# Kernel tuning notes

Measured on AMD Instinct MI355X. Metric: run time of the kernel, lower is better.

Reference implementation:

```python
import jax, jax.numpy as jnp
import numpy as np

B, S, D = 4, 2048, 2048
NQ, NKV = 16, 4
HD = D // NQ          # head_size = 128
GROUP = NQ // NKV     # 4


def _rope_table(seq_len, head_size, theta=10000.0):
    # [seq, head_size/2, 2] = (cos, sin), matching torch polar freqs_cis
    inv = 1.0 / (theta ** (np.arange(0, head_size, 2, dtype=np.float32) / head_size))
    ang = np.arange(seq_len, dtype=np.float32)[:, None] * inv[None, :]
    return jnp.asarray(np.stack([np.cos(ang), np.sin(ang)], axis=-1))


def setup_inputs() -> dict:
    key = jax.random.key(0)
    ks = jax.random.split(key, 6)
    sd = 0.02
    return {
        "x": jax.random.normal(ks[0], (B, S, D), jnp.float32),
        "freq_cis": _rope_table(S, HD),
        "Wq": jax.random.normal(ks[1], (D, NQ * HD), jnp.float32) * sd,
        "bq": jnp.zeros((NQ * HD,), jnp.float32),
        "Wk": jax.random.normal(ks[2], (D, NKV * HD), jnp.float32) * sd,
        "bk": jnp.zeros((NKV * HD,), jnp.float32),
        "Wv": jax.random.normal(ks[3], (D, NKV * HD), jnp.float32) * sd,
        "bv": jnp.zeros((NKV * HD,), jnp.float32),
        "Wo": jax.random.normal(ks[4], (NQ * HD, D), jnp.float32) * sd,
        "start_pos": 0,
    }


def _apply_rope(x, fc):
    # x: [b, s, h, d]; fc: [s, d/2, 2] -> complex multiply on (even, odd) pairs
    xr = x.reshape(*x.shape[:-1], -1, 2)
    cos = fc[None, :, None, :, 0]
    sin = fc[None, :, None, :, 1]
    x0, x1 = xr[..., 0], xr[..., 1]
    out = jnp.stack([x0 * cos - x1 * sin, x0 * sin + x1 * cos], axis=-1)
    return out.reshape(x.shape)


def reference(x, freq_cis, Wq, bq, Wk, bk, Wv, bv, Wo, start_pos):
    b, s, _ = x.shape
    q = (x @ Wq + bq).reshape(b, s, NQ, HD)
    k = (x @ Wk + bk).reshape(b, s, NKV, HD)
    v = (x @ Wv + bv).reshape(b, s, NKV, HD)

    fc = freq_cis[start_pos:start_pos + s]
    q = _apply_rope(q, fc)
    k = _apply_rope(k, fc)

    # [b, nkv, group, s, d] query view; k/v stay [b, nkv, s, d] (GQA broadcast)
    q = q.transpose(0, 2, 1, 3).reshape(b, NKV, GROUP, s, HD)
    k = k.transpose(0, 2, 1, 3)
    v = v.transpose(0, 2, 1, 3)

    scale = 1.0 / jnp.sqrt(jnp.asarray(HD, x.dtype))
    scores = jnp.einsum("bhgqd,bhkd->bhgqk", q, k) * scale
    causal = jnp.tril(jnp.ones((s, s), bool))
    scores = jnp.where(causal[None, None, None], scores, jnp.asarray(-jnp.inf, scores.dtype))
    probs = jax.nn.softmax(scores, axis=-1)
    o = jnp.einsum("bhgqk,bhkd->bhgqd", probs, v)

    o = o.reshape(b, NQ, s, HD).transpose(0, 2, 1, 3).reshape(b, s, NQ * HD)
    return o @ Wo
```

## Files before the change

kernel.cpp:

```cpp
#include <hip/hip_runtime.h>
#include <stdint.h>

typedef __attribute__((ext_vector_type(8))) short bf16x8;
typedef __attribute__((ext_vector_type(4))) float f32x4;
typedef __attribute__((ext_vector_type(16))) float f32x16;

#define S_LEN 2048
#define D_MODEL 2048
#define NQH 16
#define NKVH 4
#define HDIM 128
#define BATCH 4

__device__ __forceinline__ float bf2f(unsigned short s) {
  union { unsigned u; float f; } v; v.u = ((unsigned)s) << 16; return v.f;
}
__device__ __forceinline__ unsigned short f2bf(float f) {
  union { float f; unsigned u; } v; v.f = f;
  unsigned r = v.u + 0x7FFFu + ((v.u >> 16) & 1u);
  return (unsigned short)(r >> 16);
}
__device__ __forceinline__ f32x4 fzero() {
  f32x4 v; v[0]=0.f; v[1]=0.f; v[2]=0.f; v[3]=0.f; return v;
}
__device__ __forceinline__ void async16(const void* g, void* l) {
  __builtin_amdgcn_global_load_lds(
      (const __attribute__((address_space(1))) unsigned int*)g,
      (__attribute__((address_space(3))) unsigned int*)l, 16, 0, 0);
}
__device__ __forceinline__ unsigned cvtpk(float lo, float hi) {
  unsigned r;
  asm("v_cvt_pk_bf16_f32 %0, %1, %2" : "=v"(r) : "v"(lo), "v"(hi));
  return r;
}

__global__ void k_convert_x(const float* __restrict__ x, unsigned short* __restrict__ xb, int n4) {
  int stride = gridDim.x * blockDim.x;
  for (int i = blockIdx.x * blockDim.x + threadIdx.x; i < n4; i += stride) {
    float4 v = ((const float4*)x)[i];
    ushort4 o;
    o.x = f2bf(v.x); o.y = f2bf(v.y); o.z = f2bf(v.z); o.w = f2bf(v.w);
    ((ushort4*)xb)[i] = o;
  }
}

__global__ void k_transpose_convert(const float* __restrict__ W, unsigned short* __restrict__ Wt,
                                    int K, int N) {
  __shared__ float tile[32][33];
  int tx = threadIdx.x & 31, ty = threadIdx.x >> 5;
  int n0 = blockIdx.x * 32, k0 = blockIdx.y * 32;
  #pragma unroll
  for (int i = 0; i < 4; ++i)
    tile[ty + i*8][tx] = W[(size_t)(k0 + ty + i*8) * N + n0 + tx];
  __syncthreads();
  #pragma unroll
  for (int i = 0; i < 4; ++i)
    Wt[(size_t)(n0 + ty + i*8) * K + k0 + tx] = f2bf(tile[tx][ty + i*8]);
}

__global__ void k_transpose_bf16(const unsigned short* __restrict__ src,
                                 unsigned short* __restrict__ dst, int R, int C) {
  __shared__ unsigned short tile[32][33];
  int tx = threadIdx.x & 31, ty = threadIdx.x >> 5;
  int c0 = blockIdx.x * 32, r0 = blockIdx.y * 32;
  const unsigned short* s = src + (size_t)blockIdx.z * R * C;
  unsigned short* d = dst + (size_t)blockIdx.z * R * C;
  #pragma unroll
  for (int i = 0; i < 4; ++i)
    tile[ty + i*8][tx] = s[(size_t)(r0 + ty + i*8) * C + c0 + tx];
  __syncthreads();
  #pragma unroll
  for (int i = 0; i < 4; ++i)
    d[(size_t)(c0 + ty + i*8) * R + r0 + tx] = tile[tx][ty + i*8];
}

__global__ void k_rope(unsigned short* __restrict__ T, const float* __restrict__ fc,
                       const int* __restrict__ start_pos, int total) {
  int sp = start_pos[0];
  int stride = gridDim.x * blockDim.x;
  for (int i = blockIdx.x * blockDim.x + threadIdx.x; i < total; i += stride) {
    int d2 = i & 63;
    int s = (i >> 6) & (S_LEN - 1);
    unsigned v = ((const unsigned*)T)[i];
    float x0 = bf2f((unsigned short)(v & 0xFFFFu));
    float x1 = bf2f((unsigned short)(v >> 16));
    float c  = fc[((size_t)(sp + s) * 64 + d2) * 2];
    float sn = fc[((size_t)(sp + s) * 64 + d2) * 2 + 1];
    float y0 = x0 * c - x1 * sn;
    float y1 = x0 * sn + x1 * c;
    ((unsigned*)T)[i] = (unsigned)f2bf(y0) | ((unsigned)f2bf(y1) << 16);
  }
}

__global__ __launch_bounds__(256) void k_gemm_qkv(
    const unsigned short* __restrict__ A, const unsigned short* __restrict__ Bt,
    const float* __restrict__ bq, const float* __restrict__ bk, const float* __restrict__ bv,
    unsigned short* __restrict__ Qo, unsigned short* __restrict__ Ko, unsigned short* __restrict__ Vo)
{
  const int Kdim = 2048;
  __shared__ unsigned short As[128 * 64];
  __shared__ unsigned short Bs[128 * 64];
  const int tid = threadIdx.x;
  const int lane = tid & 63, wave = tid >> 6;
  const int lr = lane & 15, g = lane >> 4;
  const int wm = wave >> 1, wn = wave & 1;
  const int mbase = blockIdx.y * 128;
  const int nbase = blockIdx.x * 128;

  f32x4 acc[4][4];
  #pragma unroll
  for (int mr = 0; mr < 4; ++mr)
    #pragma unroll
    for (int nr = 0; nr < 4; ++nr) acc[mr][nr] = fzero();

  for (int kt = 0; kt < Kdim / 64; ++kt) {
    #pragma unroll
    for (int it = 0; it < 4; ++it) {
      int c = tid + it * 256;
      int row = c >> 3, col = c & 7;
      int lcol = col ^ (row & 7);
      async16(A + (size_t)(mbase + row) * Kdim + kt * 64 + lcol * 8, &As[c * 8]);
    }
    #pragma unroll
    for (int it = 0; it < 4; ++it) {
      int c = tid + it * 256;
      int row = c >> 3, col = c & 7;
      int lcol = col ^ (row & 7);
      async16(Bt + (size_t)(nbase + row) * Kdim + kt * 64 + lcol * 8, &Bs[c * 8]);
    }
    __syncthreads();
    #pragma unroll
    for (int kc = 0; kc < 2; ++kc) {
      bf16x8 af[4], bfr[4];
      int Xl = kc * 64 + g * 16;
      #pragma unroll
      for (int mr = 0; mr < 4; ++mr) {
        int row = wm * 64 + mr * 16 + lr;
        int Xs = Xl ^ ((row & 7) << 4);
        af[mr] = *(const bf16x8*)&As[row * 64 + Xs / 2];
      }
      #pragma unroll
      for (int nr = 0; nr < 4; ++nr) {
        int row = wn * 64 + nr * 16 + lr;
        int Xs = Xl ^ ((row & 7) << 4);
        bfr[nr] = *(const bf16x8*)&Bs[row * 64 + Xs / 2];
      }
      #pragma unroll
      for (int mr = 0; mr < 4; ++mr)
        #pragma unroll
        for (int nr = 0; nr < 4; ++nr)
          acc[mr][nr] = __builtin_amdgcn_mfma_f32_16x16x32_bf16(af[mr], bfr[nr], acc[mr][nr], 0, 0, 0);
    }
    __syncthreads();
  }

  #pragma unroll
  for (int mr = 0; mr < 4; ++mr)
    #pragma unroll
    for (int nr = 0; nr < 4; ++nr)
      #pragma unroll
      for (int i = 0; i < 4; ++i) {
        int m = mbase + wm * 64 + mr * 16 + g * 4 + i;
        int n = nbase + wn * 64 + nr * 16 + lr;
        int b = m >> 11, s = m & 2047;
        float val = acc[mr][nr][i];
        if (n < 2048) {
          val += bq[n];
          int h = n >> 7, d = n & 127;
          Qo[((size_t)(b * NQH + h) * S_LEN + s) * HDIM + d] = f2bf(val);
        } else if (n < 2560) {
          int nn = n - 2048;
          val += bk[nn];
          int h = nn >> 7, d = nn & 127;
          Ko[((size_t)(b * NKVH + h) * S_LEN + s) * HDIM + d] = f2bf(val);
        } else {
          int nn = n - 2560;
          val += bv[nn];
          int h = nn >> 7, d = nn & 127;
          Vo[((size_t)(b * NKVH + h) * S_LEN + s) * HDIM + d] = f2bf(val);
        }
      }
}

__global__ __launch_bounds__(256) void k_gemm_out(
    const unsigned short* __restrict__ A, const unsigned short* __restrict__ Bt,
    float* __restrict__ C)
{
  const int Kdim = 2048;
  __shared__ unsigned short As[128 * 64];
  __shared__ unsigned short Bs[128 * 64];
  const int tid = threadIdx.x;
  const int lane = tid & 63, wave = tid >> 6;
  const int lr = lane & 15, g = lane >> 4;
  const int wm = wave >> 1, wn = wave & 1;
  const int mbase = blockIdx.y * 128;
  const int nbase = blockIdx.x * 128;

  f32x4 acc[4][4];
  #pragma unroll
  for (int mr = 0; mr < 4; ++mr)
    #pragma unroll
    for (int nr = 0; nr < 4; ++nr) acc[mr][nr] = fzero();

  for (int kt = 0; kt < Kdim / 64; ++kt) {
    #pragma unroll
    for (int it = 0; it < 4; ++it) {
      int c = tid + it * 256;
      int row = c >> 3, col = c & 7;
      int lcol = col ^ (row & 7);
      async16(A + (size_t)(mbase + row) * Kdim + kt * 64 + lcol * 8, &As[c * 8]);
    }
    #pragma unroll
    for (int it = 0; it < 4; ++it) {
      int c = tid + it * 256;
      int row = c >> 3, col = c & 7;
      int lcol = col ^ (row & 7);
      async16(Bt + (size_t)(nbase + row) * Kdim + kt * 64 + lcol * 8, &Bs[c * 8]);
    }
    __syncthreads();
    #pragma unroll
    for (int kc = 0; kc < 2; ++kc) {
      bf16x8 af[4], bfr[4];
      int Xl = kc * 64 + g * 16;
      #pragma unroll
      for (int mr = 0; mr < 4; ++mr) {
        int row = wm * 64 + mr * 16 + lr;
        int Xs = Xl ^ ((row & 7) << 4);
        af[mr] = *(const bf16x8*)&As[row * 64 + Xs / 2];
      }
      #pragma unroll
      for (int nr = 0; nr < 4; ++nr) {
        int row = wn * 64 + nr * 16 + lr;
        int Xs = Xl ^ ((row & 7) << 4);
        bfr[nr] = *(const bf16x8*)&Bs[row * 64 + Xs / 2];
      }
      #pragma unroll
      for (int mr = 0; mr < 4; ++mr)
        #pragma unroll
        for (int nr = 0; nr < 4; ++nr)
          acc[mr][nr] = __builtin_amdgcn_mfma_f32_16x16x32_bf16(af[mr], bfr[nr], acc[mr][nr], 0, 0, 0);
    }
    __syncthreads();
  }

  #pragma unroll
  for (int mr = 0; mr < 4; ++mr)
    #pragma unroll
    for (int nr = 0; nr < 4; ++nr)
      #pragma unroll
      for (int i = 0; i < 4; ++i) {
        int m = mbase + wm * 64 + mr * 16 + g * 4 + i;
        int n = nbase + wn * 64 + nr * 16 + lr;
        C[(size_t)m * 2048 + n] = acc[mr][nr][i];
      }
}

__global__ __launch_bounds__(512, 2) void k_flash2(
    const unsigned short* __restrict__ Q, const unsigned short* __restrict__ K,
    const unsigned short* __restrict__ Vt, unsigned short* __restrict__ O)
{
  __shared__ __align__(16) unsigned short SH[32768];

  const int tid = threadIdx.x;
  const int lane = tid & 63;
  const int w = tid >> 6;
  const int ql = lane & 31;
  const int hi = lane >> 5;

  const int bh = blockIdx.x >> 2;
  const int tp = blockIdx.x & 3;
  const int b = bh >> 4, h = bh & 15;
  const int kh = h >> 2;

  const unsigned short* Qbase = Q + (size_t)(b * NQH + h) * S_LEN * HDIM;
  const unsigned short* Kbase = K + (size_t)(b * NKVH + kh) * S_LEN * HDIM;
  const unsigned short* Vtb   = Vt + (size_t)(b * NKVH + kh) * HDIM * S_LEN;

  const float scale = 0.08838834764831845f;

  #pragma unroll 1
  for (int half = 0; half < 2; ++half) {
    const int t = half ? (7 - tp) : tp;
    const int nkv = 4 * t + 4;
    const int qg = t * 256 + w * 32 + ql;

    __syncthreads();

    bf16x8 qf[8];
    {
      const unsigned short* qp = Qbase + (size_t)qg * HDIM;
      #pragma unroll
      for (int dd = 0; dd < 8; ++dd)
        qf[dd] = *(const bf16x8*)(qp + dd * 16 + hi * 8);
    }

    float m_r = -1e30f, l_r = 0.f;
    f32x16 oA[4];
    #pragma unroll
    for (int db = 0; db < 4; ++db)
      #pragma unroll
      for (int r = 0; r < 16; ++r) oA[db][r] = 0.f;

    {
      unsigned short* Kd = SH;
      unsigned short* Vd = SH + 16384;
      #pragma unroll
      for (int it = 0; it < 2; ++it) {
        int c = tid + it * 512;
        int row = c >> 4, col = c & 15;
        int lcol = (col & 8) | ((col ^ (row & 7)) & 7);
        async16(Kbase + (size_t)row * HDIM + lcol * 8, Kd + c * 8);
      }
      #pragma unroll
      for (int it = 0; it < 2; ++it) {
        int c = tid + it * 512;
        int row = c >> 3, col = c & 7;
        int lcol = col ^ (row & 7);
        async16(Vtb + (size_t)row * S_LEN + lcol * 8, Vd + c * 8);
      }
    }
    __syncthreads();

    for (int j = 0; j < nkv; ++j) {
      const int cur = j & 1;
      const unsigned short* Kl = SH + cur * 8192;
      const unsigned short* Vl = SH + 16384 + cur * 8192;

      if (j + 1 < nkv) {
        unsigned short* Kd = SH + (cur ^ 1) * 8192;
        unsigned short* Vd = SH + 16384 + (cur ^ 1) * 8192;
        #pragma unroll
        for (int it = 0; it < 2; ++it) {
          int c = tid + it * 512;
          int row = c >> 4, col = c & 15;
          int lcol = (col & 8) | ((col ^ (row & 7)) & 7);
          async16(Kbase + (size_t)((j + 1) * 64 + row) * HDIM + lcol * 8, Kd + c * 8);
        }
        #pragma unroll
        for (int it = 0; it < 2; ++it) {
          int c = tid + it * 512;
          int row = c >> 3, col = c & 7;
          int lcol = col ^ (row & 7);
          async16(Vtb + (size_t)row * S_LEN + (j + 1) * 64 + lcol * 8, Vd + c * 8);
        }
      }

      if (j * 64 <= t * 256 + w * 32 + 31) {
        f32x16 p0, p1;
        #pragma unroll
        for (int r = 0; r < 16; ++r) { p0[r] = 0.f; p1[r] = 0.f; }
        #pragma unroll
        for (int dd = 0; dd < 8; ++dd) {
          const int off = (((dd * 32 + hi * 16) ^ ((ql & 7) << 4)) >> 1);
          bf16x8 a0 = *(const bf16x8*)&Kl[ql * 128 + off];
          bf16x8 a1 = *(const bf16x8*)&Kl[(32 + ql) * 128 + off];
          p0 = __builtin_amdgcn_mfma_f32_32x32x16_bf16(a0, qf[dd], p0, 0, 0, 0);
          p1 = __builtin_amdgcn_mfma_f32_32x32x16_bf16(a1, qf[dd], p1, 0, 0, 0);
        }

        #pragma unroll
        for (int r = 0; r < 16; ++r) {
          const int kl = (r & 3) + 8 * (r >> 2);
          int kg = j * 64 + kl + 4 * hi;
          p0[r] = (kg > qg) ? -1e30f : p0[r] * scale;
          p1[r] = (kg + 32 > qg) ? -1e30f : p1[r] * scale;
        }

        float pm = -1e30f;
        #pragma unroll
        for (int r = 0; r < 16; ++r) pm = fmaxf(pm, fmaxf(p0[r], p1[r]));
        pm = fmaxf(pm, __shfl_xor(pm, 32));
        const float mn = fmaxf(m_r, pm);
        const float corr = __expf(m_r - mn);
        m_r = mn;
        float rs = 0.f;
        #pragma unroll
        for (int r = 0; r < 16; ++r) {
          p0[r] = __expf(p0[r] - mn);
          p1[r] = __expf(p1[r] - mn);
          rs += p0[r] + p1[r];
        }
        rs += __shfl_xor(rs, 32);
        l_r = l_r * corr + rs;
        #pragma unroll
        for (int db = 0; db < 4; ++db)
          #pragma unroll
          for (int r = 0; r < 16; ++r) oA[db][r] *= corr;

        bf16x8 pb[4];
        {
          unsigned Wv[8], W2v[8];
          #pragma unroll
          for (int d = 0; d < 4; ++d) {
            Wv[d]      = cvtpk(p0[4*d],     p0[4*d + 1]);
            W2v[d]     = cvtpk(p0[4*d + 2], p0[4*d + 3]);
            Wv[4 + d]  = cvtpk(p1[4*d],     p1[4*d + 1]);
            W2v[4 + d] = cvtpk(p1[4*d + 2], p1[4*d + 3]);
          }
          #pragma unroll
          for (int kt = 0; kt < 2; ++kt) {
            #pragma unroll
            for (int s = 0; s < 2; ++s) {
              unsigned ownW   = hi ? Wv[kt*4 + 2*s + 1]  : Wv[kt*4 + 2*s];
              unsigned sendW  = hi ? Wv[kt*4 + 2*s]      : Wv[kt*4 + 2*s + 1];
              unsigned recvW  = (unsigned)__shfl_xor((int)sendW, 32);
              unsigned ownW2  = hi ? W2v[kt*4 + 2*s + 1] : W2v[kt*4 + 2*s];
              unsigned sendW2 = hi ? W2v[kt*4 + 2*s]     : W2v[kt*4 + 2*s + 1];
              unsigned recvW2 = (unsigned)__shfl_xor((int)sendW2, 32);
              union { unsigned u[4]; bf16x8 v; } pk;
              pk.u[0] = hi ? recvW  : ownW;
              pk.u[1] = hi ? recvW2 : ownW2;
              pk.u[2] = hi ? ownW   : recvW;
              pk.u[3] = hi ? ownW2  : recvW2;
              pb[kt*2 + s] = pk.v;
            }
          }
        }

        #pragma unroll
        for (int ks = 0; ks < 4; ++ks) {
          #pragma unroll
          for (int db = 0; db < 4; ++db) {
            const int off = (((ks * 32 + hi * 16) ^ ((ql & 7) << 4)) >> 1);
            bf16x8 av = *(const bf16x8*)&Vl[(db * 32 + ql) * 64 + off];
            oA[db] = __builtin_amdgcn_mfma_f32_32x32x16_bf16(av, pb[ks], oA[db], 0, 0, 0);
          }
        }
      }
      __syncthreads();
    }

    {
      const float invl = 1.f / l_r;
      const int qloc = w * 32 + ql;
      #pragma unroll
      for (int db = 0; db < 4; ++db)
        #pragma unroll
        for (int g4 = 0; g4 < 4; ++g4) {
          unsigned lo  = cvtpk(oA[db][g4*4 + 0] * invl, oA[db][g4*4 + 1] * invl);
          unsigned hi2 = cvtpk(oA[db][g4*4 + 2] * invl, oA[db][g4*4 + 3] * invl);
          int byteoff = qloc * 256 + ((db * 64 + g4 * 16 + hi * 8) ^ ((qloc & 7) << 4));
          *(uint2*)((char*)SH + byteoff) = make_uint2(lo, hi2);
        }
    }
    __syncthreads();
    {
      const int q2 = tid >> 1, hf = tid & 1;
      unsigned short* orow = O + ((size_t)(b * S_LEN + t * 256 + q2)) * D_MODEL + h * HDIM + hf * 64;
      #pragma unroll
      for (int u = 0; u < 8; ++u) {
        int byteoff = q2 * 256 + ((hf * 128 + u * 16) ^ ((q2 & 7) << 4));
        bf16x8 v = *(const bf16x8*)((const char*)SH + byteoff);
        *(bf16x8*)(orow + u * 8) = v;
      }
    }
  }
}

extern "C" void kernel_launch(void* const* d_in, const int* in_sizes, int n_in,
                              void* d_out, int out_size, void* d_ws, size_t ws_size,
                              hipStream_t stream) {
  (void)in_sizes; (void)n_in; (void)out_size; (void)ws_size;
  const float* x  = (const float*)d_in[0];
  const float* fc = (const float*)d_in[1];
  const float* Wq = (const float*)d_in[2];
  const float* bq = (const float*)d_in[3];
  const float* Wk = (const float*)d_in[4];
  const float* bk = (const float*)d_in[5];
  const float* Wv = (const float*)d_in[6];
  const float* bv = (const float*)d_in[7];
  const float* Wo = (const float*)d_in[8];
  const int* start_pos = (const int*)d_in[9];
  float* out = (float*)d_out;

  unsigned short* ws = (unsigned short*)d_ws;
  size_t off = 0;
  unsigned short* xb  = ws + off; off += (size_t)8192 * 2048;
  unsigned short* Wt  = ws + off; off += (size_t)3072 * 2048;
  unsigned short* Wot = ws + off; off += (size_t)2048 * 2048;
  unsigned short* Qb  = ws + off; off += (size_t)BATCH * NQH  * S_LEN * HDIM;
  unsigned short* Kb  = ws + off; off += (size_t)BATCH * NKVH * S_LEN * HDIM;
  unsigned short* Vb  = ws + off; off += (size_t)BATCH * NKVH * S_LEN * HDIM;
  unsigned short* Vtb = ws + off; off += (size_t)BATCH * NKVH * S_LEN * HDIM;
  unsigned short* Ob  = ws + off; off += (size_t)8192 * 2048;

  k_convert_x<<<2048, 256, 0, stream>>>(x, xb, 8192 * 2048 / 4);
  k_transpose_convert<<<dim3(64, 64), 256, 0, stream>>>(Wq, Wt, 2048, 2048);
  k_transpose_convert<<<dim3(16, 64), 256, 0, stream>>>(Wk, Wt + (size_t)2048 * 2048, 2048, 512);
  k_transpose_convert<<<dim3(16, 64), 256, 0, stream>>>(Wv, Wt + (size_t)2560 * 2048, 2048, 512);
  k_transpose_convert<<<dim3(64, 64), 256, 0, stream>>>(Wo, Wot, 2048, 2048);

  k_gemm_qkv<<<dim3(24, 64), 256, 0, stream>>>(xb, Wt, bq, bk, bv, Qb, Kb, Vb);

  k_rope<<<2048, 256, 0, stream>>>(Qb, fc, start_pos, BATCH * NQH * S_LEN * 64);
  k_rope<<<2048, 256, 0, stream>>>(Kb, fc, start_pos, BATCH * NKVH * S_LEN * 64);
  k_transpose_bf16<<<dim3(4, 64, 16), 256, 0, stream>>>(Vb, Vtb, S_LEN, HDIM);

  k_flash2<<<dim3(256), 512, 0, stream>>>(Qb, Kb, Vtb, Ob);

  k_gemm_out<<<dim3(16, 64), 256, 0, stream>>>(Ob, Wot, out);
}
```

Measured before the change: 398.2 us.

## Replace QKV and output GEMMs with 256x256 double-buffered pipelined GEMM

Replaces both 128x128 single-buffered GEMM kernels with one templated 256x256-tile kernel using 8 waves. It double-buffers LDS and splits each K-step into four quarter phases that interleave async global-to-LDS staging with MFMA work, using manual waitcnt, barriers and setprio. It also remaps block IDs so neighbouring workgroups share A/B tiles in cache. Larger tiles raise data reuse but leave fewer workgroups (384 and 256) to fill the CUs. The hand-written wait counts are fragile and could race if they are wrong.

```diff
diff --git a/kernel.cpp b/kernel.cpp
--- a/kernel.cpp
+++ b/kernel.cpp
@@ -92,167 +92,181 @@
   }
 }
 
-__global__ __launch_bounds__(256) void k_gemm_qkv(
+
+__device__ __forceinline__ bf16x8 ldsrd(const unsigned short* L, int row, int kk, int g) {
+  int Xs = (kk * 64 + g * 16) ^ ((row & 7) << 4);
+  return *(const bf16x8*)&L[row * 64 + (Xs >> 1)];
+}
+__device__ __forceinline__ void stage8(const unsigned short* __restrict__ G, int gbase,
+                                       int k0, unsigned short* lds, int rowbase, int lane) {
+  int row = rowbase + (lane >> 3);
+  int col8 = (lane & 7) ^ ((lane >> 3) & 7);
+  async16(G + (size_t)(gbase + row) * 2048 + k0 + col8 * 8, lds + rowbase * 64 + lane * 8);
+}
+
+#define BARRIER() __builtin_amdgcn_s_barrier()
+#define LGKM0()  do { asm volatile("s_waitcnt lgkmcnt(0)" ::: "memory"); \
+                      __builtin_amdgcn_sched_barrier(0); } while (0)
+#define VMCNT4() asm volatile("s_waitcnt vmcnt(4)" ::: "memory")
+
+template<int EPI>
+__global__ __launch_bounds__(512, 2) void k_gemm256(
     const unsigned short* __restrict__ A, const unsigned short* __restrict__ Bt,
     const float* __restrict__ bq, const float* __restrict__ bk, const float* __restrict__ bv,
-    unsigned short* __restrict__ Qo, unsigned short* __restrict__ Ko, unsigned short* __restrict__ Vo)
+    unsigned short* __restrict__ Qo, unsigned short* __restrict__ Ko, unsigned short* __restrict__ Vo,
+    float* __restrict__ Cf, int NXT)
 {
-  const int Kdim = 2048;
-  __shared__ unsigned short As[128 * 64];
-  __shared__ unsigned short Bs[128 * 64];
-  const int tid = threadIdx.x;
-  const int lane = tid & 63, wave = tid >> 6;
+  __shared__ __align__(16) unsigned short Abuf[2][256 * 64];
+  __shared__ __align__(16) unsigned short Bbuf[2][256 * 64];
+  const int NT = 32;
+  const int tid = threadIdx.x, lane = tid & 63, w = tid >> 6;
   const int lr = lane & 15, g = lane >> 4;
-  const int wm = wave >> 1, wn = wave & 1;
-  const int mbase = blockIdx.y * 128;
-  const int nbase = blockIdx.x * 128;
-
-  f32x4 acc[4][4];
+  const int wm = w >> 2, wn = w & 3;
+
+  int nwg = NXT * 32;
+  int cpx = nwg >> 3;
+  int bid = blockIdx.x;
+  int swz = (bid & 7) * cpx + (bid >> 3);
+  const int by = swz / NXT, bx = swz % NXT;
+  const int mbase = by * 256, nbase = bx * 256;
+
+  #define ST_AQ02(tt) if ((tt) < NT) { unsigned short* L = Abuf[(tt) & 1]; int k0 = (tt) * 64; \
+    _Pragma("unroll") for (int it = 0; it < 2; ++it) { int sub = it * 8 + w; \
+      stage8(A, mbase, k0, L, (sub >> 3) * 128 + (sub & 7) * 8, lane); } }
+  #define ST_AQ13(tt) if ((tt) < NT) { unsigned short* L = Abuf[(tt) & 1]; int k0 = (tt) * 64; \
+    _Pragma("unroll") for (int it = 0; it < 2; ++it) { int sub = it * 8 + w; \
+      stage8(A, mbase, k0, L, 64 + (sub >> 3) * 128 + (sub & 7) * 8, lane); } }
+  #define ST_BS0(tt) if ((tt) < NT) { unsigned short* L = Bbuf[(tt) & 1]; int k0 = (tt) * 64; \
+    _Pragma("unroll") for (int it = 0; it < 2; ++it) { int sub = it * 8 + w; \
+      stage8(Bt, nbase, k0, L, (sub >> 2) * 64 + (sub & 3) * 8, lane); } }
+  #define ST_BS1(tt) if ((tt) < NT) { unsigned short* L = Bbuf[(tt) & 1]; int k0 = (tt) * 64; \
+    _Pragma("unroll") for (int it = 0; it < 2; ++it) { int sub = it * 8 + w; \
+      stage8(Bt, nbase, k0, L, 32 + (sub >> 2) * 64 + (sub & 3) * 8, lane); } }
+
+  f32x4 acc[8][4];
   #pragma unroll
-  for (int mr = 0; mr < 4; ++mr)
-    #pragma unroll
-    for (int nr = 0; nr < 4; ++nr) acc[mr][nr] = fzero();
-
-  for (int kt = 0; kt < Kdim / 64; ++kt) {
-    #pragma unroll
-    for (int it = 0; it < 4; ++it) {
-      int c = tid + it * 256;
-      int row = c >> 3, col = c & 7;
-      int lcol = col ^ (row & 7);
-      async16(A + (size_t)(mbase + row) * Kdim + kt * 64 + lcol * 8, &As[c * 8]);
+  for (int m = 0; m < 8; ++m)
+    #pragma unroll
+    for (int n = 0; n < 4; ++n) acc[m][n] = fzero();
+
+  ST_AQ02(0); ST_AQ13(0); ST_BS0(0); ST_BS1(0);
+  ST_AQ02(1); ST_BS1(1);
+  VMCNT4();
+  BARRIER();
+
+  bf16x8 a[2][4], b[2][2];
+
+  for (int t = 0; t < NT; ++t) {
+    const unsigned short* Al = Abuf[t & 1];
+    const unsigned short* Bl = Bbuf[t & 1];
+
+    #pragma unroll
+    for (int kk = 0; kk < 2; ++kk) {
+      #pragma unroll
+      for (int m = 0; m < 4; ++m) a[kk][m] = ldsrd(Al, wm * 128 + m * 16 + lr, kk, g);
+      #pragma unroll
+      for (int n = 0; n < 2; ++n) b[kk][n] = ldsrd(Bl, wn * 64 + n * 16 + lr, kk, g);
     }
-    #pragma unroll
-    for (int it = 0; it < 4; ++it) {
-      int c = tid + it * 256;
-      int row = c >> 3, col = c & 7;
-      int lcol = col ^ (row & 7);
-      async16(Bt + (size_t)(nbase + row) * Kdim + kt * 64 + lcol * 8, &Bs[c * 8]);
-    }
-    __syncthreads();
-    #pragma unroll
-    for (int kc = 0; kc < 2; ++kc) {
-      bf16x8 af[4], bfr[4];
-      int Xl = kc * 64 + g * 16;
-      #pragma unroll
-      for (int mr = 0; mr < 4; ++mr) {
-        int row = wm * 64 + mr * 16 + lr;
-        int Xs = Xl ^ ((row & 7) << 4);
-        af[mr] = *(const bf16x8*)&As[row * 64 + Xs / 2];
+    ST_AQ13(t + 1);
+    BARRIER(); LGKM0();
+    __builtin_amdgcn_s_setprio(1);
+    #pragma unroll
+    for (int kk = 0; kk < 2; ++kk)
+      #pragma unroll
+      for (int m = 0; m < 4; ++m)
+        #pragma unroll
+        for (int n = 0; n < 2; ++n)
+          acc[m][n] = __builtin_amdgcn_mfma_f32_16x16x32_bf16(a[kk][m], b[kk][n], acc[m][n], 0, 0, 0);
+    __builtin_amdgcn_s_setprio(0);
+    BARRIER();
+
+    #pragma unroll
+    for (int kk = 0; kk < 2; ++kk)
+      #pragma unroll
+      for (int n = 0; n < 2; ++n) b[kk][n] = ldsrd(Bl, wn * 64 + (2 + n) * 16 + lr, kk, g);
+    ST_BS0(t + 1);
+    BARRIER(); LGKM0();
+    __builtin_amdgcn_s_setprio(1);
+    #pragma unroll
+    for (int kk = 0; kk < 2; ++kk)
+      #pragma unroll
+      for (int m = 0; m < 4; ++m)
+        #pragma unroll
+        for (int n = 0; n < 2; ++n)
+          acc[m][2 + n] = __builtin_amdgcn_mfma_f32_16x16x32_bf16(a[kk][m], b[kk][n], acc[m][2 + n], 0, 0, 0);
+    __builtin_amdgcn_s_setprio(0);
+    BARRIER();
+
+    #pragma unroll
+    for (int kk = 0; kk < 2; ++kk)
+      #pragma unroll
+      for (int m = 0; m < 4; ++m) a[kk][m] = ldsrd(Al, wm * 128 + 64 + m * 16 + lr, kk, g);
+    ST_AQ02(t + 2);
+    BARRIER(); LGKM0();
+    __builtin_amdgcn_s_setprio(1);
+    #pragma unroll
+    for (int kk = 0; kk < 2; ++kk)
+      #pragma unroll
+      for (int m = 0; m < 4; ++m)
+        #pragma unroll
+        for (int n = 0; n < 2; ++n)
+          acc[4 + m][2 + n] = __builtin_amdgcn_mfma_f32_16x16x32_bf16(a[kk][m], b[kk][n], acc[4 + m][2 + n], 0, 0, 0);
+    __builtin_amdgcn_s_setprio(0);
+    BARRIER();
+
+    #pragma unroll
+    for (int kk = 0; kk < 2; ++kk)
+      #pragma unroll
+      for (int n = 0; n < 2; ++n) b[kk][n] = ldsrd(Bl, wn * 64 + n * 16 + lr, kk, g);
+    ST_BS1(t + 2);
+    VMCNT4();
+    BARRIER(); LGKM0();
+    __builtin_amdgcn_s_setprio(1);
+    #pragma unroll
+    for (int kk = 0; kk < 2; ++kk)
+      #pragma unroll
+      for (int m = 0; m < 4; ++m)
+        #pragma unroll
+        for (int n = 0; n < 2; ++n)
+          acc[4 + m][n] = __builtin_amdgcn_mfma_f32_16x16x32_bf16(a[kk][m], b[kk][n], acc[4 + m][n], 0, 0, 0);
+    __builtin_amdgcn_s_setprio(0);
+    BARRIER();
+  }
+
+  #pragma unroll
+  for (int m = 0; m < 8; ++m)
+    #pragma unroll
+    for (int n = 0; n < 4; ++n)
+      #pragma unroll
+      for (int i = 0; i < 4; ++i) {
+        int mg = mbase + wm * 128 + m * 16 + g * 4 + i;
+        int ng = nbase + wn * 64 + n * 16 + lr;
+        float val = acc[m][n][i];
+        if (EPI == 1) {
+          Cf[(size_t)mg * 2048 + ng] = val;
+        } else {
+          int bb = mg >> 11, s = mg & 2047;
+          if (ng < 2048) {
+            val += bq[ng];
+            int h = ng >> 7, d = ng & 127;
+            Qo[((size_t)(bb * NQH + h) * S_LEN + s) * HDIM + d] = f2bf(val);
+          } else if (ng < 2560) {
+            int nn = ng - 2048;
+            val += bk[nn];
+            int h = nn >> 7, d = nn & 127;
+            Ko[((size_t)(bb * NKVH + h) * S_LEN + s) * HDIM + d] = f2bf(val);
+          } else {
+            int nn = ng - 2560;
+            val += bv[nn];
+            int h = nn >> 7, d = nn & 127;
+            Vo[((size_t)(bb * NKVH + h) * S_LEN + s) * HDIM + d] = f2bf(val);
+          }
+        }
       }
-      #pragma unroll
-      for (int nr = 0; nr < 4; ++nr) {
-        int row = wn * 64 + nr * 16 + lr;
-        int Xs = Xl ^ ((row & 7) << 4);
-        bfr[nr] = *(const bf16x8*)&Bs[row * 64 + Xs / 2];
-      }
-      #pragma unroll
-      for (int mr = 0; mr < 4; ++mr)
-        #pragma unroll
-        for (int nr = 0; nr < 4; ++nr)
-          acc[mr][nr] = __builtin_amdgcn_mfma_f32_16x16x32_bf16(af[mr], bfr[nr], acc[mr][nr], 0, 0, 0);
-    }
-    __syncthreads();
-  }
-
-  #pragma unroll
-  for (int mr = 0; mr < 4; ++mr)
-    #pragma unroll
-    for (int nr = 0; nr < 4; ++nr)
-      #pragma unroll
-      for (int i = 0; i < 4; ++i) {
-        int m = mbase + wm * 64 + mr * 16 + g * 4 + i;
-        int n = nbase + wn * 64 + nr * 16 + lr;
-        int b = m >> 11, s = m & 2047;
-        float val = acc[mr][nr][i];
-        if (n < 2048) {
-          val += bq[n];
-          int h = n >> 7, d = n & 127;
-          Qo[((size_t)(b * NQH + h) * S_LEN + s) * HDIM + d] = f2bf(val);
-        } else if (n < 2560) {
-          int nn = n - 2048;
-          val += bk[nn];
-          int h = nn >> 7, d = nn & 127;
-          Ko[((size_t)(b * NKVH + h) * S_LEN + s) * HDIM + d] = f2bf(val);
-        } else {
-          int nn = n - 2560;
-          val += bv[nn];
-          int h = nn >> 7, d = nn & 127;
-          Vo[((size_t)(b * NKVH + h) * S_LEN + s) * HDIM + d] = f2bf(val);
-        }
-      }
-}
-
-__global__ __launch_bounds__(256) void k_gemm_out(
-    const unsigned short* __restrict__ A, const unsigned short* __restrict__ Bt,
-    float* __restrict__ C)
-{
-  const int Kdim = 2048;
-  __shared__ unsigned short As[128 * 64];
-  __shared__ unsigned short Bs[128 * 64];
-  const int tid = threadIdx.x;
-  const int lane = tid & 63, wave = tid >> 6;
-  const int lr = lane & 15, g = lane >> 4;
-  const int wm = wave >> 1, wn = wave & 1;
-  const int mbase = blockIdx.y * 128;
-  const int nbase = blockIdx.x * 128;
-
-  f32x4 acc[4][4];
-  #pragma unroll
-  for (int mr = 0; mr < 4; ++mr)
-    #pragma unroll
-    for (int nr = 0; nr < 4; ++nr) acc[mr][nr] = fzero();
-
-  for (int kt = 0; kt < Kdim / 64; ++kt) {
-    #pragma unroll
-    for (int it = 0; it < 4; ++it) {
-      int c = tid + it * 256;
-      int row = c >> 3, col = c & 7;
-      int lcol = col ^ (row & 7);
-      async16(A + (size_t)(mbase + row) * Kdim + kt * 64 + lcol * 8, &As[c * 8]);
-    }
-    #pragma unroll
-    for (int it = 0; it < 4; ++it) {
-      int c = tid + it * 256;
-      int row = c >> 3, col = c & 7;
-      int lcol = col ^ (row & 7);
-      async16(Bt + (size_t)(nbase + row) * Kdim + kt * 64 + lcol * 8, &Bs[c * 8]);
-    }
-    __syncthreads();
-    #pragma unroll
-    for (int kc = 0; kc < 2; ++kc) {
-      bf16x8 af[4], bfr[4];
-      int Xl = kc * 64 + g * 16;
-      #pragma unroll
-      for (int mr = 0; mr < 4; ++mr) {
-        int row = wm * 64 + mr * 16 + lr;
-        int Xs = Xl ^ ((row & 7) << 4);
-        af[mr] = *(const bf16x8*)&As[row * 64 + Xs / 2];
-      }
-      #pragma unroll
-      for (int nr = 0; nr < 4; ++nr) {
-        int row = wn * 64 + nr * 16 + lr;
-        int Xs = Xl ^ ((row & 7) << 4);
-        bfr[nr] = *(const bf16x8*)&Bs[row * 64 + Xs / 2];
-      }
-      #pragma unroll
-      for (int mr = 0; mr < 4; ++mr)
-        #pragma unroll
-        for (int nr = 0; nr < 4; ++nr)
-          acc[mr][nr] = __builtin_amdgcn_mfma_f32_16x16x32_bf16(af[mr], bfr[nr], acc[mr][nr], 0, 0, 0);
-    }
-    __syncthreads();
-  }
-
-  #pragma unroll
-  for (int mr = 0; mr < 4; ++mr)
-    #pragma unroll
-    for (int nr = 0; nr < 4; ++nr)
-      #pragma unroll
-      for (int i = 0; i < 4; ++i) {
-        int m = mbase + wm * 64 + mr * 16 + g * 4 + i;
-        int n = nbase + wn * 64 + nr * 16 + lr;
-        C[(size_t)m * 2048 + n] = acc[mr][nr][i];
-      }
+  #undef ST_AQ02
+  #undef ST_AQ13
+  #undef ST_BS0
+  #undef ST_BS1
 }
 
 __global__ __launch_bounds__(512, 2) void k_flash2(
@@ -490,7 +504,7 @@
   k_transpose_convert<<<dim3(16, 64), 256, 0, stream>>>(Wv, Wt + (size_t)2560 * 2048, 2048, 512);
   k_transpose_convert<<<dim3(64, 64), 256, 0, stream>>>(Wo, Wot, 2048, 2048);
 
-  k_gemm_qkv<<<dim3(24, 64), 256, 0, stream>>>(xb, Wt, bq, bk, bv, Qb, Kb, Vb);
+  k_gemm256<0><<<dim3(384), 512, 0, stream>>>(xb, Wt, bq, bk, bv, Qb, Kb, Vb, nullptr, 12);
 
   k_rope<<<2048, 256, 0, stream>>>(Qb, fc, start_pos, BATCH * NQH * S_LEN * 64);
   k_rope<<<2048, 256, 0, stream>>>(Kb, fc, start_pos, BATCH * NKVH * S_LEN * 64);
@@ -498,5 +512,6 @@
 
   k_flash2<<<dim3(256), 512, 0, stream>>>(Qb, Kb, Vtb, Ob);
 
-  k_gemm_out<<<dim3(16, 64), 256, 0, stream>>>(Ob, Wot, out);
-}
+  k_gemm256<1><<<dim3(256), 512, 0, stream>>>(Ob, Wot, nullptr, nullptr, nullptr,
+                                              nullptr, nullptr, nullptr, out, 8);
+}
```

Result: faster. 385.8 us (-3.1%).
